# Kernel optimization log

Hardware: AMD Instinct MI355X
Metric: run time of the kernel (lower is better)

## Reference

```python
import jax, jax.numpy as jnp
import numpy as np

B, L, H, NB, D, DH = 8, 4096, 16, 8, 1024, 128

def setup_inputs() -> dict:
    key = jax.random.key(0)
    ks = jax.random.split(key, 12)
    theta_path = jax.random.normal(ks[0], (B, L, H, NB), jnp.float32)
    content_emb = jax.random.normal(ks[1], (B, L, D), jnp.float32)
    s_in = 1.0 / np.sqrt(D).astype(np.float32)
    s_h = 1.0 / np.sqrt(DH).astype(np.float32)
    # log_R_head: Linear(D,128) -> GELU -> Linear(128, H*NB), last layer weight *0.01, bias 0
    r_w1 = jax.random.normal(ks[2], (D, DH), jnp.float32) * s_in
    r_b1 = jnp.zeros((DH,), jnp.float32)
    r_w2 = jax.random.normal(ks[3], (DH, H * NB), jnp.float32) * s_h * 0.01
    r_b2 = jnp.zeros((H * NB,), jnp.float32)
    # measure_head
    m_w1 = jax.random.normal(ks[4], (D, DH), jnp.float32) * s_in
    m_b1 = jax.random.normal(ks[5], (DH,), jnp.float32) * s_in
    m_w2 = jax.random.normal(ks[6], (DH, H * NB), jnp.float32) * s_h
    m_b2 = jax.random.normal(ks[7], (H * NB,), jnp.float32) * s_h
    log_Q = jnp.full((H, NB), -3.0, jnp.float32)
    log_R_avg = jnp.full((H, NB), 1.0, jnp.float32)
    return {"theta_path": theta_path, "content_emb": content_emb,
            "log_Q": log_Q, "log_R_avg": log_R_avg,
            "r_w1": r_w1, "r_b1": r_b1, "r_w2": r_w2, "r_b2": r_b2,
            "m_w1": m_w1, "m_b1": m_b1, "m_w2": m_w2, "m_b2": m_b2}

def _mlp(x, w1, b1, w2, b2):
    h = jax.nn.gelu(x @ w1 + b1, approximate=False)  # torch nn.GELU default = exact
    return h @ w2 + b2

def reference(theta_path, content_emb, log_Q, log_R_avg,
              r_w1, r_b1, r_w2, r_b2, m_w1, m_b1, m_w2, m_b2):
    b, l, h, nb = theta_path.shape
    log_R = jnp.clip(_mlp(content_emb, r_w1, r_b1, r_w2, r_b2).reshape(b, l, h, nb), -5.0, 5.0)
    R = jnp.exp(log_R)
    z = jnp.pi * jnp.tanh(_mlp(content_emb, m_w1, m_b1, m_w2, m_b2).reshape(b, l, h, nb))
    diff = z - theta_path
    nu = jnp.arctan2(jnp.sin(diff), jnp.cos(diff))  # wrap angle error to (-pi, pi]
    Q = jnp.exp(log_Q)
    Ravg = jnp.exp(log_R_avg)
    Pi_dare = 0.5 * (-Q + jnp.sqrt(Q * Q + 4.0 * Q * Ravg))  # [H, NB]
    Pi = jnp.broadcast_to(Pi_dare[None, None], (b, l, h, nb))
    K = Pi / jnp.maximum(Pi + R, 1e-8)
    alpha = 1.0 - K
    u = K * nu
    # affine associative scan over sequence dim: d_t = alpha_t * d_{t-1} + u_t
    def combine(c1, c2):
        a1, u1 = c1
        a2, u2 = c2
        return (a2 * a1, a2 * u1 + u2)
    _, d = jax.lax.associative_scan(combine, (alpha, u), axis=1)
    return (theta_path + d, Pi, K, R)
```

## Files before the change

### kernel.cpp

```cpp
#include <hip/hip_runtime.h>
#include <hip/hip_bf16.h>
#include <cstdint>
#include <cstddef>

#define TOK 32768
#define CCH 128
#define DIN 1024

typedef __attribute__((ext_vector_type(8))) short short8;
typedef __attribute__((ext_vector_type(4))) float f32x4;

#define LIST_CAP 262144u

static __device__ __forceinline__ uint16_t f2bf(float f) {
  __hip_bfloat16 h = __float2bfloat16(f);
  return __builtin_bit_cast(uint16_t, h);
}
static __device__ __forceinline__ float bf2f(uint16_t u) {
  __hip_bfloat16 h = __builtin_bit_cast(__hip_bfloat16, u);
  return __bfloat162float(h);
}
static __device__ __forceinline__ void splitbf(float x, uint16_t& hi, uint16_t& lo) {
  hi = f2bf(x);
  lo = f2bf(x - bf2f(hi));
}

__global__ void prep_kernel(const float* __restrict__ r_w1, const float* __restrict__ r_w2,
                            const float* __restrict__ m_w1, const float* __restrict__ m_w2,
                            const float* __restrict__ logQ, const float* __restrict__ logRavg,
                            uint16_t* __restrict__ W1r, uint16_t* __restrict__ W2r,
                            uint16_t* __restrict__ W1mh, uint16_t* __restrict__ W1ml,
                            uint16_t* __restrict__ W2mh, uint16_t* __restrict__ W2ml,
                            float* __restrict__ PiArr, unsigned int* __restrict__ cnt)
{
  int idx = blockIdx.x * 256 + threadIdx.x;
  if (idx == 0) cnt[0] = 0;
  if (idx < 131072) {
    int e = idx;
    int j = e & 7, lane = (e >> 3) & 63, nt = (e >> 9) & 7, c = (e >> 12) & 1, kt = e >> 13;
    int k = kt * 64 + c * 32 + (lane >> 4) * 8 + j;
    int n = nt * 16 + (lane & 15);
    W1r[e] = f2bf(r_w1[k * 128 + n]);
  } else if (idx < 147456) {
    int e = idx - 131072;
    int j = e & 7, l = (e >> 3) & 63, c = (e >> 9) & 3, t = e >> 11;
    int k = c * 32 + (l >> 4) * 8 + j;
    int col = t * 16 + (l & 15);
    W2r[e] = f2bf(r_w2[k * 128 + col]);
  } else if (idx < 278528) {
    int e = idx - 147456;
    int j = e & 7, lane = (e >> 3) & 63, nt = (e >> 9) & 7, c = (e >> 12) & 1, kt = e >> 13;
    int k = kt * 64 + c * 32 + (lane >> 4) * 8 + j;
    int n = nt * 16 + (lane & 15);
    uint16_t h, l;
    splitbf(m_w1[k * 128 + n], h, l);
    W1mh[e] = h; W1ml[e] = l;
  } else if (idx < 294912) {
    int e = idx - 278528;
    int j = e & 7, l = (e >> 3) & 63, c = (e >> 9) & 3, t = e >> 11;
    int k = c * 32 + (l >> 4) * 8 + j;
    int col = t * 16 + (l & 15);
    uint16_t h, lo;
    splitbf(m_w2[k * 128 + col], h, lo);
    W2mh[e] = h; W2ml[e] = lo;
  } else if (idx < 295040) {
    int i = idx - 294912;
    float Q = expf(logQ[i]);
    float Rv = expf(logRavg[i]);
    PiArr[i] = 0.5f * (-Q + sqrtf(Q * Q + 4.0f * Q * Rv));
  }
}

__global__ __launch_bounds__(1024, 8) void fused_all(
    const float* __restrict__ X, const float* __restrict__ theta,
    const uint16_t* __restrict__ W1r, const uint16_t* __restrict__ W2r,
    const uint16_t* __restrict__ W1h, const uint16_t* __restrict__ W1l,
    const uint16_t* __restrict__ W2h, const uint16_t* __restrict__ W2l,
    const float* __restrict__ rB1, const float* __restrict__ rB2,
    const float* __restrict__ B1, const float* __restrict__ B2,
    const float* __restrict__ PiArr,
    float* __restrict__ out0, float* __restrict__ out1,
    float* __restrict__ out2, float* __restrict__ out3,
    float* __restrict__ AggA, float* __restrict__ AggU,
    unsigned int* __restrict__ cnt, unsigned int* __restrict__ list)
{
  union SM {
    struct { uint16_t Xh[2][64][72]; uint16_t Xl[2][64][72]; } s1;
    struct { uint16_t Hh[64][136]; uint16_t Hl[64][136]; uint16_t Hr[64][136]; } s2;
    struct { float2 Agg[4][4][128]; } s3;
  };
  __shared__ SM sm;

  const int tid = threadIdx.x;
  const int w = tid >> 6, lane = tid & 63;
  const int l15 = lane & 15, l4 = lane >> 4;
  const int tm = w >> 2, tn = w & 3;
  const int tok0 = blockIdx.x * 64;

  f32x4 accm[2], accr[2];
#pragma unroll
  for (int t = 0; t < 2; ++t) { accm[t] = 0.0f; accr[t] = 0.0f; }

  const int rr = tid >> 4, cc = tid & 15;
  float4 xv0;

  auto stageLoad = [&](int kt) {
    xv0 = *reinterpret_cast<const float4*>(
        X + (size_t)(tok0 + rr) * DIN + kt * 64 + cc * 4);
  };
  auto stageWrite = [&](int b) {
    ushort4 vh, vl;
    splitbf(xv0.x, vh.x, vl.x);
    splitbf(xv0.y, vh.y, vl.y);
    splitbf(xv0.z, vh.z, vl.z);
    splitbf(xv0.w, vh.w, vl.w);
    *reinterpret_cast<ushort4*>(&sm.s1.Xh[b][rr][cc * 4]) = vh;
    *reinterpret_cast<ushort4*>(&sm.s1.Xl[b][rr][cc * 4]) = vl;
  };

  stageLoad(0);
  stageWrite(0);
  __syncthreads();

  for (int kt = 0; kt < 16; ++kt) {
    const int cur = kt & 1;
    if (kt < 15) stageLoad(kt + 1);

    short8 bh[2][2], bl[2][2], br[2][2];
#pragma unroll
    for (int c = 0; c < 2; ++c)
#pragma unroll
      for (int t = 0; t < 2; ++t) {
        const size_t boff = (size_t)((((kt * 2 + c) * 8 + (tn * 2 + t)) * 64 + lane) * 8);
        bh[c][t] = *reinterpret_cast<const short8*>(W1h + boff);
        bl[c][t] = *reinterpret_cast<const short8*>(W1l + boff);
        br[c][t] = *reinterpret_cast<const short8*>(W1r + boff);
      }

#pragma unroll
    for (int c = 0; c < 2; ++c) {
      const int ko = c * 32 + l4 * 8;
      const int row = tm * 16 + l15;
      short8 ah = *reinterpret_cast<const short8*>(&sm.s1.Xh[cur][row][ko]);
      short8 al = *reinterpret_cast<const short8*>(&sm.s1.Xl[cur][row][ko]);
#pragma unroll
      for (int t = 0; t < 2; ++t) {
        accm[t] = __builtin_amdgcn_mfma_f32_16x16x32_bf16(ah, bh[c][t], accm[t], 0, 0, 0);
        accm[t] = __builtin_amdgcn_mfma_f32_16x16x32_bf16(al, bh[c][t], accm[t], 0, 0, 0);
        accm[t] = __builtin_amdgcn_mfma_f32_16x16x32_bf16(ah, bl[c][t], accm[t], 0, 0, 0);
        accr[t] = __builtin_amdgcn_mfma_f32_16x16x32_bf16(ah, br[c][t], accr[t], 0, 0, 0);
      }
    }

    if (kt < 15) stageWrite(cur ^ 1);
    __syncthreads();
  }

#pragma unroll
  for (int t = 0; t < 2; ++t) {
    const int n = (tn * 2 + t) * 16 + l15;
    const float b1m = B1[n];
    const float b1rr = rB1[n];
#pragma unroll
    for (int r = 0; r < 4; ++r) {
      const int row = tm * 16 + l4 * 4 + r;
      const float v = accm[t][r] + b1m;
      const float ev = erff(v / 1.41421356237309515f);
      const float g = 0.5f * v * (ev + 1.0f);
      uint16_t gh, gl;
      splitbf(g, gh, gl);
      sm.s2.Hh[row][n] = gh;
      sm.s2.Hl[row][n] = gl;
      const float vr = accr[t][r] + b1rr;
      const float gr = 0.5f * vr * (1.0f + erff(vr * 0.70710678118654752f));
      sm.s2.Hr[row][n] = f2bf(gr);
    }
  }
  __syncthreads();

  f32x4 acc2m[2], acc2r[2];
#pragma unroll
  for (int t = 0; t < 2; ++t) { acc2m[t] = 0.0f; acc2r[t] = 0.0f; }

#pragma unroll
  for (int c2 = 0; c2 < 4; ++c2) {
    const int ko = c2 * 32 + l4 * 8;
    const int row = tm * 16 + l15;
    short8 ah = *reinterpret_cast<const short8*>(&sm.s2.Hh[row][ko]);
    short8 al = *reinterpret_cast<const short8*>(&sm.s2.Hl[row][ko]);
    short8 ar = *reinterpret_cast<const short8*>(&sm.s2.Hr[row][ko]);
    short8 b2h[2], b2l[2], b2r[2];
#pragma unroll
    for (int t = 0; t < 2; ++t) {
      const size_t boff = (size_t)((((tn * 2 + t) * 4 + c2) * 64 + lane) * 8);
      b2h[t] = *reinterpret_cast<const short8*>(W2h + boff);
      b2l[t] = *reinterpret_cast<const short8*>(W2l + boff);
      b2r[t] = *reinterpret_cast<const short8*>(W2r + boff);
    }
#pragma unroll
    for (int t = 0; t < 2; ++t) {
      acc2m[t] = __builtin_amdgcn_mfma_f32_16x16x32_bf16(ah, b2h[t], acc2m[t], 0, 0, 0);
      acc2m[t] = __builtin_amdgcn_mfma_f32_16x16x32_bf16(al, b2h[t], acc2m[t], 0, 0, 0);
      acc2m[t] = __builtin_amdgcn_mfma_f32_16x16x32_bf16(ah, b2l[t], acc2m[t], 0, 0, 0);
      acc2r[t] = __builtin_amdgcn_mfma_f32_16x16x32_bf16(ar, b2r[t], acc2r[t], 0, 0, 0);
    }
  }

#pragma unroll
  for (int t = 0; t < 2; ++t) {
    const int n = (tn * 2 + t) * 16 + l15;
    const float b2 = rB2[n];
    const float piv = PiArr[n];
#pragma unroll
    for (int r = 0; r < 4; ++r) {
      const int token = tok0 + tm * 16 + l4 * 4 + r;
      float lr = acc2r[t][r] + b2;
      lr = fminf(fmaxf(lr, -5.0f), 5.0f);
      const float R = expf(lr);
      const float K = piv / fmaxf(piv + R, 1e-8f);
      const size_t off = (size_t)token * CCH + n;
      out1[off] = piv;
      out2[off] = K;
      out3[off] = R;
      acc2r[t][r] = K;
    }
  }

#pragma unroll
  for (int t = 0; t < 2; ++t) {
    const int n = (tn * 2 + t) * 16 + l15;
    const float b2 = B2[n];
#pragma unroll
    for (int r = 0; r < 4; ++r) {
      const int token = tok0 + tm * 16 + l4 * 4 + r;
      const float mz = acc2m[t][r] + b2;
      const float z = 3.14159265358979323846f * tanhf(mz);
      const float d = z - theta[(size_t)token * CCH + n];
      const float wr = d - 6.2831853071795864769f * rintf(d * 0.15915494309189533577f);
      if (3.14159265358979323846f - fabsf(wr) < 3e-4f) {
        unsigned int p = atomicAdd(cnt, 1u);
        if (p < LIST_CAP) list[p] = (unsigned int)(token * CCH + n);
      }
      out0[(size_t)token * CCH + n] = wr;
      acc2m[t][r] = wr;
    }
  }

  __syncthreads();
#pragma unroll
  for (int t = 0; t < 2; ++t) {
    const int n = (tn * 2 + t) * 16 + l15;
    float A = 1.0f, U = 0.0f;
#pragma unroll
    for (int r = 0; r < 4; ++r) {
      const float k = acc2r[t][r];
      const float v = acc2m[t][r];
      const float a = 1.0f - k;
      A *= a;
      U = fmaf(a, U, k * v);
    }
    sm.s3.Agg[tm][l4][n] = make_float2(A, U);
  }
  __syncthreads();
  if (tid < 128) {
    const int ch = tid;
    float A = 1.0f, U = 0.0f;
#pragma unroll
    for (int g = 0; g < 16; ++g) {
      const float2 au = sm.s3.Agg[g >> 2][g & 3][ch];
      U = fmaf(au.x, U, au.y);
      A *= au.x;
    }
    AggA[blockIdx.x * CCH + ch] = A;
    AggU[blockIdx.x * CCH + ch] = U;
  }
}

__global__ __launch_bounds__(128) void refine_nu(
    const float* __restrict__ X, const float* __restrict__ theta,
    const float* __restrict__ W1, const float* __restrict__ B1,
    const float* __restrict__ W2, const float* __restrict__ B2,
    const unsigned int* __restrict__ cnt, const unsigned int* __restrict__ list,
    float* __restrict__ out0)
{
  __shared__ float h[128];
  const int j = threadIdx.x;
  const unsigned int n = min(cnt[0], LIST_CAP);
  for (unsigned int e = blockIdx.x; e < n; e += gridDim.x) {
    const unsigned int idx = list[e];
    const int tok = (int)(idx >> 7), ch = (int)(idx & 127);
    const float* xr = X + (size_t)tok * DIN;
    float acc = 0.0f;
    for (int k = 0; k < DIN; ++k)
      acc = fmaf(xr[k], W1[(size_t)k * CCH + j], acc);
    const float v = acc + B1[j];
    const float ev = erff(v / 1.41421356237309515f);
    h[j] = 0.5f * v * (ev + 1.0f);
    __syncthreads();
    if (j == 0) {
      float a2 = 0.0f;
      for (int k = 0; k < CCH; ++k)
        a2 = fmaf(h[k], W2[(size_t)k * CCH + ch], a2);
      const float mz = a2 + B2[ch];
      const float z = 3.14159265358979323846f * tanhf(mz);
      const float d = z - theta[(size_t)tok * CCH + ch];
      out0[(size_t)tok * CCH + ch] = atan2f(sinf(d), cosf(d));
    }
    __syncthreads();
  }
}

__global__ __launch_bounds__(64) void refine_agg(
    const float* __restrict__ Kk, const float* __restrict__ nu,
    const unsigned int* __restrict__ cnt, const unsigned int* __restrict__ list,
    float* __restrict__ AggA, float* __restrict__ AggU)
{
  __shared__ float av[64], uv[64];
  const int i = threadIdx.x;
  const unsigned int n = min(cnt[0], LIST_CAP);
  for (unsigned int e = blockIdx.x; e < n; e += gridDim.x) {
    const unsigned int idx = list[e];
    const int ch = (int)(idx & 127);
    const int blk = (int)(idx >> 13);
    const size_t off = (size_t)(blk * 64 + i) * CCH + ch;
    const float k = Kk[off];
    const float v = nu[off];
    av[i] = 1.0f - k;
    uv[i] = k * v;
    __syncthreads();
    if (i == 0) {
      float A = 1.0f, U = 0.0f;
      for (int g = 0; g < 64; ++g) {
        U = fmaf(av[g], U, uv[g]);
        A *= av[g];
      }
      AggA[blk * CCH + ch] = A;
      AggU[blk * CCH + ch] = U;
    }
    __syncthreads();
  }
}

__global__ __launch_bounds__(256) void scan_pass2(
    const float* __restrict__ AggA, const float* __restrict__ AggU,
    float* __restrict__ Carry)
{
  const int wid = blockIdx.x * 4 + (threadIdx.x >> 6);
  const int b = wid >> 7, ch = wid & 127;
  const int g = threadIdx.x & 63;
  const size_t idx = (size_t)(b * 64 + g) * CCH + ch;
  float A = AggA[idx];
  float U = AggU[idx];
#pragma unroll
  for (int s = 1; s < 64; s <<= 1) {
    const float pA = __shfl_up(A, s);
    const float pU = __shfl_up(U, s);
    if (g >= s) {
      U = fmaf(A, pU, U);
      A = A * pA;
    }
  }
  float cU = __shfl_up(U, 1);
  if (g == 0) cU = 0.0f;
  Carry[idx] = cU;
}

__global__ __launch_bounds__(128) void scan_pass3(
    const float* __restrict__ Kk, const float* __restrict__ theta,
    const float* __restrict__ Carry, float* __restrict__ out0)
{
  __shared__ float kb[64 * CCH];
  __shared__ float vb[64 * CCH];
  const int c = threadIdx.x;
  const int blk = blockIdx.x;
  const size_t base = (size_t)blk * 64 * CCH;
#pragma unroll
  for (int i = 0; i < 16; ++i) {
    const int e = i * 128 + c;
    reinterpret_cast<float4*>(kb)[e] = reinterpret_cast<const float4*>(Kk + base)[e];
    reinterpret_cast<float4*>(vb)[e] = reinterpret_cast<const float4*>(out0 + base)[e];
  }
  __syncthreads();
  float d = Carry[blk * CCH + c];
#pragma unroll 8
  for (int i = 0; i < 64; ++i) {
    const float k = kb[i * CCH + c];
    const float v = vb[i * CCH + c];
    d = fmaf(1.0f - k, d, k * v);
    const size_t off = base + (size_t)i * CCH + c;
    out0[off] = theta[off] + d;
  }
}

extern "C" void kernel_launch(void* const* d_in, const int* in_sizes, int n_in,
                              void* d_out, int out_size, void* d_ws, size_t ws_size,
                              hipStream_t stream) {
  const float* theta   = (const float*)d_in[0];
  const float* X       = (const float*)d_in[1];
  const float* logQ    = (const float*)d_in[2];
  const float* logRavg = (const float*)d_in[3];
  const float* r_w1    = (const float*)d_in[4];
  const float* r_b1    = (const float*)d_in[5];
  const float* r_w2    = (const float*)d_in[6];
  const float* r_b2    = (const float*)d_in[7];
  const float* m_w1    = (const float*)d_in[8];
  const float* m_b1    = (const float*)d_in[9];
  const float* m_w2    = (const float*)d_in[10];
  const float* m_b2    = (const float*)d_in[11];

  float* out0 = (float*)d_out;
  float* out1 = out0 + 4194304;
  float* out2 = out0 + 2 * 4194304;
  float* out3 = out0 + 3 * 4194304;

  char* ws = (char*)d_ws;
  uint16_t* W1r  = (uint16_t*)(ws);
  uint16_t* W2r  = (uint16_t*)(ws + 262144);
  float* PiArr   = (float*)(ws + 295936);
  float* AggA    = (float*)(ws + 296448);
  float* AggU    = (float*)(ws + 558592);
  float* Carry   = (float*)(ws + 820736);
  unsigned int* cnt  = (unsigned int*)(ws + 1082880);
  unsigned int* list = (unsigned int*)(ws + 1083136);
  uint16_t* W1mh = (uint16_t*)(ws + 2131712);
  uint16_t* W1ml = (uint16_t*)(ws + 2393856);
  uint16_t* W2mh = (uint16_t*)(ws + 2656000);
  uint16_t* W2ml = (uint16_t*)(ws + 2688768);

  prep_kernel<<<1153, 256, 0, stream>>>(r_w1, r_w2, m_w1, m_w2, logQ, logRavg,
                                        W1r, W2r, W1mh, W1ml, W2mh, W2ml,
                                        PiArr, cnt);
  fused_all<<<512, 1024, 0, stream>>>(X, theta, W1r, W2r, W1mh, W1ml, W2mh, W2ml,
                                      r_b1, r_b2, m_b1, m_b2, PiArr,
                                      out0, out1, out2, out3, AggA, AggU, cnt, list);
  refine_nu<<<1024, 128, 0, stream>>>(X, theta, m_w1, m_b1, m_w2, m_b2,
                                      cnt, list, out0);
  refine_agg<<<1024, 64, 0, stream>>>(out2, out0, cnt, list, AggA, AggU);
  scan_pass2<<<256, 256, 0, stream>>>(AggA, AggU, Carry);
  scan_pass3<<<512, 128, 0, stream>>>(out2, theta, Carry, out0);
}
```

Before: 140.7 us.

## Remap fused MLP to 8 waves each owning one N-tile across all rows

```diff
diff --git a/kernel.cpp b/kernel.cpp
--- a/kernel.cpp
+++ b/kernel.cpp
@@ -71,7 +71,7 @@
   }
 }
 
-__global__ __launch_bounds__(1024, 8) void fused_all(
+__global__ __launch_bounds__(512, 4) void fused_all(
     const float* __restrict__ X, const float* __restrict__ theta,
     const uint16_t* __restrict__ W1r, const uint16_t* __restrict__ W2r,
     const uint16_t* __restrict__ W1h, const uint16_t* __restrict__ W1l,
@@ -94,172 +94,181 @@
   const int tid = threadIdx.x;
   const int w = tid >> 6, lane = tid & 63;
   const int l15 = lane & 15, l4 = lane >> 4;
-  const int tm = w >> 2, tn = w & 3;
+  const int tn = w;
   const int tok0 = blockIdx.x * 64;
 
-  f32x4 accm[2], accr[2];
-#pragma unroll
-  for (int t = 0; t < 2; ++t) { accm[t] = 0.0f; accr[t] = 0.0f; }
+  f32x4 accm[4], accr[4];
+#pragma unroll
+  for (int m = 0; m < 4; ++m) { accm[m] = 0.0f; accr[m] = 0.0f; }
 
   const int rr = tid >> 4, cc = tid & 15;
-  float4 xv0;
-
-  auto stageLoad = [&](int kt) {
-    xv0 = *reinterpret_cast<const float4*>(
+  float4 xa0, xa1, xb0, xb1;
+
+  auto ldX = [&](int kt, float4& v0, float4& v1) {
+    v0 = *reinterpret_cast<const float4*>(
         X + (size_t)(tok0 + rr) * DIN + kt * 64 + cc * 4);
+    v1 = *reinterpret_cast<const float4*>(
+        X + (size_t)(tok0 + rr + 32) * DIN + kt * 64 + cc * 4);
   };
-  auto stageWrite = [&](int b) {
+  auto wrX = [&](int b, const float4& v0, const float4& v1) {
     ushort4 vh, vl;
-    splitbf(xv0.x, vh.x, vl.x);
-    splitbf(xv0.y, vh.y, vl.y);
-    splitbf(xv0.z, vh.z, vl.z);
-    splitbf(xv0.w, vh.w, vl.w);
+    splitbf(v0.x, vh.x, vl.x);
+    splitbf(v0.y, vh.y, vl.y);
+    splitbf(v0.z, vh.z, vl.z);
+    splitbf(v0.w, vh.w, vl.w);
     *reinterpret_cast<ushort4*>(&sm.s1.Xh[b][rr][cc * 4]) = vh;
     *reinterpret_cast<ushort4*>(&sm.s1.Xl[b][rr][cc * 4]) = vl;
+    splitbf(v1.x, vh.x, vl.x);
+    splitbf(v1.y, vh.y, vl.y);
+    splitbf(v1.z, vh.z, vl.z);
+    splitbf(v1.w, vh.w, vl.w);
+    *reinterpret_cast<ushort4*>(&sm.s1.Xh[b][rr + 32][cc * 4]) = vh;
+    *reinterpret_cast<ushort4*>(&sm.s1.Xl[b][rr + 32][cc * 4]) = vl;
   };
 
-  stageLoad(0);
-  stageWrite(0);
+  ldX(0, xa0, xa1);
+  wrX(0, xa0, xa1);
+  ldX(1, xa0, xa1);
   __syncthreads();
 
+#pragma unroll
   for (int kt = 0; kt < 16; ++kt) {
     const int cur = kt & 1;
-    if (kt < 15) stageLoad(kt + 1);
-
-    short8 bh[2][2], bl[2][2], br[2][2];
-#pragma unroll
-    for (int c = 0; c < 2; ++c)
-#pragma unroll
-      for (int t = 0; t < 2; ++t) {
-        const size_t boff = (size_t)((((kt * 2 + c) * 8 + (tn * 2 + t)) * 64 + lane) * 8);
-        bh[c][t] = *reinterpret_cast<const short8*>(W1h + boff);
-        bl[c][t] = *reinterpret_cast<const short8*>(W1l + boff);
-        br[c][t] = *reinterpret_cast<const short8*>(W1r + boff);
-      }
+
+    short8 bh[2], bl[2], br[2];
+#pragma unroll
+    for (int c = 0; c < 2; ++c) {
+      const size_t boff = (size_t)((((kt * 2 + c) * 8 + tn) * 64 + lane) * 8);
+      bh[c] = *reinterpret_cast<const short8*>(W1h + boff);
+      bl[c] = *reinterpret_cast<const short8*>(W1l + boff);
+      br[c] = *reinterpret_cast<const short8*>(W1r + boff);
+    }
+    if (kt < 14) ldX(kt + 2, xb0, xb1);
 
 #pragma unroll
     for (int c = 0; c < 2; ++c) {
       const int ko = c * 32 + l4 * 8;
-      const int row = tm * 16 + l15;
-      short8 ah = *reinterpret_cast<const short8*>(&sm.s1.Xh[cur][row][ko]);
-      short8 al = *reinterpret_cast<const short8*>(&sm.s1.Xl[cur][row][ko]);
-#pragma unroll
-      for (int t = 0; t < 2; ++t) {
-        accm[t] = __builtin_amdgcn_mfma_f32_16x16x32_bf16(ah, bh[c][t], accm[t], 0, 0, 0);
-        accm[t] = __builtin_amdgcn_mfma_f32_16x16x32_bf16(al, bh[c][t], accm[t], 0, 0, 0);
-        accm[t] = __builtin_amdgcn_mfma_f32_16x16x32_bf16(ah, bl[c][t], accm[t], 0, 0, 0);
-        accr[t] = __builtin_amdgcn_mfma_f32_16x16x32_bf16(ah, br[c][t], accr[t], 0, 0, 0);
+#pragma unroll
+      for (int m = 0; m < 4; ++m) {
+        const int row = m * 16 + l15;
+        const short8 ah = *reinterpret_cast<const short8*>(&sm.s1.Xh[cur][row][ko]);
+        const short8 al = *reinterpret_cast<const short8*>(&sm.s1.Xl[cur][row][ko]);
+        accm[m] = __builtin_amdgcn_mfma_f32_16x16x32_bf16(ah, bh[c], accm[m], 0, 0, 0);
+        accm[m] = __builtin_amdgcn_mfma_f32_16x16x32_bf16(al, bh[c], accm[m], 0, 0, 0);
+        accm[m] = __builtin_amdgcn_mfma_f32_16x16x32_bf16(ah, bl[c], accm[m], 0, 0, 0);
+        accr[m] = __builtin_amdgcn_mfma_f32_16x16x32_bf16(ah, br[c], accr[m], 0, 0, 0);
       }
     }
 
-    if (kt < 15) stageWrite(cur ^ 1);
+    if (kt < 15) { wrX(cur ^ 1, xa0, xa1); xa0 = xb0; xa1 = xb1; }
     __syncthreads();
   }
 
-#pragma unroll
-  for (int t = 0; t < 2; ++t) {
-    const int n = (tn * 2 + t) * 16 + l15;
+  short8 b2h[4], b2l[4], b2r[4];
+#pragma unroll
+  for (int c2 = 0; c2 < 4; ++c2) {
+    const size_t boff = (size_t)(((tn * 4 + c2) * 64 + lane) * 8);
+    b2h[c2] = *reinterpret_cast<const short8*>(W2h + boff);
+    b2l[c2] = *reinterpret_cast<const short8*>(W2l + boff);
+    b2r[c2] = *reinterpret_cast<const short8*>(W2r + boff);
+  }
+
+  const int n = tn * 16 + l15;
+  {
     const float b1m = B1[n];
     const float b1rr = rB1[n];
 #pragma unroll
-    for (int r = 0; r < 4; ++r) {
-      const int row = tm * 16 + l4 * 4 + r;
-      const float v = accm[t][r] + b1m;
-      const float ev = erff(v / 1.41421356237309515f);
-      const float g = 0.5f * v * (ev + 1.0f);
-      uint16_t gh, gl;
-      splitbf(g, gh, gl);
-      sm.s2.Hh[row][n] = gh;
-      sm.s2.Hl[row][n] = gl;
-      const float vr = accr[t][r] + b1rr;
-      const float gr = 0.5f * vr * (1.0f + erff(vr * 0.70710678118654752f));
-      sm.s2.Hr[row][n] = f2bf(gr);
-    }
+    for (int m = 0; m < 4; ++m)
+#pragma unroll
+      for (int r = 0; r < 4; ++r) {
+        const int row = m * 16 + l4 * 4 + r;
+        const float v = accm[m][r] + b1m;
+        const float ev = erff(v / 1.41421356237309515f);
+        const float g = 0.5f * v * (ev + 1.0f);
+        uint16_t gh, gl;
+        splitbf(g, gh, gl);
+        sm.s2.Hh[row][n] = gh;
+        sm.s2.Hl[row][n] = gl;
+        const float vr = accr[m][r] + b1rr;
+        const float gr = 0.5f * vr * (1.0f + erff(vr * 0.70710678118654752f));
+        sm.s2.Hr[row][n] = f2bf(gr);
+      }
   }
   __syncthreads();
 
-  f32x4 acc2m[2], acc2r[2];
-#pragma unroll
-  for (int t = 0; t < 2; ++t) { acc2m[t] = 0.0f; acc2r[t] = 0.0f; }
+  f32x4 acc2m[4], acc2r[4];
+#pragma unroll
+  for (int m = 0; m < 4; ++m) { acc2m[m] = 0.0f; acc2r[m] = 0.0f; }
 
 #pragma unroll
   for (int c2 = 0; c2 < 4; ++c2) {
     const int ko = c2 * 32 + l4 * 8;
-    const int row = tm * 16 + l15;
-    short8 ah = *reinterpret_cast<const short8*>(&sm.s2.Hh[row][ko]);
-    short8 al = *reinterpret_cast<const short8*>(&sm.s2.Hl[row][ko]);
-    short8 ar = *reinterpret_cast<const short8*>(&sm.s2.Hr[row][ko]);
-    short8 b2h[2], b2l[2], b2r[2];
-#pragma unroll
-    for (int t = 0; t < 2; ++t) {
-      const size_t boff = (size_t)((((tn * 2 + t) * 4 + c2) * 64 + lane) * 8);
-      b2h[t] = *reinterpret_cast<const short8*>(W2h + boff);
-      b2l[t] = *reinterpret_cast<const short8*>(W2l + boff);
-      b2r[t] = *reinterpret_cast<const short8*>(W2r + boff);
-    }
-#pragma unroll
-    for (int t = 0; t < 2; ++t) {
-      acc2m[t] = __builtin_amdgcn_mfma_f32_16x16x32_bf16(ah, b2h[t], acc2m[t], 0, 0, 0);
-      acc2m[t] = __builtin_amdgcn_mfma_f32_16x16x32_bf16(al, b2h[t], acc2m[t], 0, 0, 0);
-      acc2m[t] = __builtin_amdgcn_mfma_f32_16x16x32_bf16(ah, b2l[t], acc2m[t], 0, 0, 0);
-      acc2r[t] = __builtin_amdgcn_mfma_f32_16x16x32_bf16(ar, b2r[t], acc2r[t], 0, 0, 0);
-    }
-  }
-
-#pragma unroll
-  for (int t = 0; t < 2; ++t) {
-    const int n = (tn * 2 + t) * 16 + l15;
+#pragma unroll
+    for (int m = 0; m < 4; ++m) {
+      const int row = m * 16 + l15;
+      const short8 ah = *reinterpret_cast<const short8*>(&sm.s2.Hh[row][ko]);
+      const short8 al = *reinterpret_cast<const short8*>(&sm.s2.Hl[row][ko]);
+      const short8 ar = *reinterpret_cast<const short8*>(&sm.s2.Hr[row][ko]);
+      acc2m[m] = __builtin_amdgcn_mfma_f32_16x16x32_bf16(ah, b2h[c2], acc2m[m], 0, 0, 0);
+      acc2m[m] = __builtin_amdgcn_mfma_f32_16x16x32_bf16(al, b2h[c2], acc2m[m], 0, 0, 0);
+      acc2m[m] = __builtin_amdgcn_mfma_f32_16x16x32_bf16(ah, b2l[c2], acc2m[m], 0, 0, 0);
+      acc2r[m] = __builtin_amdgcn_mfma_f32_16x16x32_bf16(ar, b2r[c2], acc2r[m], 0, 0, 0);
+    }
+  }
+
+  {
     const float b2 = rB2[n];
     const float piv = PiArr[n];
 #pragma unroll
+    for (int m = 0; m < 4; ++m)
+#pragma unroll
+      for (int r = 0; r < 4; ++r) {
+        const int token = tok0 + m * 16 + l4 * 4 + r;
+        float lr = acc2r[m][r] + b2;
+        lr = fminf(fmaxf(lr, -5.0f), 5.0f);
+        const float R = expf(lr);
+        const float K = piv / fmaxf(piv + R, 1e-8f);
+        const size_t off = (size_t)token * CCH + n;
+        out1[off] = piv;
+        out2[off] = K;
+        out3[off] = R;
+        acc2r[m][r] = K;
+      }
+  }
+
+  {
+    const float b2 = B2[n];
+#pragma unroll
+    for (int m = 0; m < 4; ++m)
+#pragma unroll
+      for (int r = 0; r < 4; ++r) {
+        const int token = tok0 + m * 16 + l4 * 4 + r;
+        const float mz = acc2m[m][r] + b2;
+        const float z = 3.14159265358979323846f * tanhf(mz);
+        const float d = z - theta[(size_t)token * CCH + n];
+        const float wr = d - 6.2831853071795864769f * rintf(d * 0.15915494309189533577f);
+        if (3.14159265358979323846f - fabsf(wr) < 3e-4f) {
+          unsigned int p = atomicAdd(cnt, 1u);
+          if (p < LIST_CAP) list[p] = (unsigned int)(token * CCH + n);
+        }
+        out0[(size_t)token * CCH + n] = wr;
+        acc2m[m][r] = wr;
+      }
+  }
+
+  __syncthreads();
+#pragma unroll
+  for (int m = 0; m < 4; ++m) {
+    float A = 1.0f, U = 0.0f;
+#pragma unroll
     for (int r = 0; r < 4; ++r) {
-      const int token = tok0 + tm * 16 + l4 * 4 + r;
-      float lr = acc2r[t][r] + b2;
-      lr = fminf(fmaxf(lr, -5.0f), 5.0f);
-      const float R = expf(lr);
-      const float K = piv / fmaxf(piv + R, 1e-8f);
-      const size_t off = (size_t)token * CCH + n;
-      out1[off] = piv;
-      out2[off] = K;
-      out3[off] = R;
-      acc2r[t][r] = K;
-    }
-  }
-
-#pragma unroll
-  for (int t = 0; t < 2; ++t) {
-    const int n = (tn * 2 + t) * 16 + l15;
-    const float b2 = B2[n];
-#pragma unroll
-    for (int r = 0; r < 4; ++r) {
-      const int token = tok0 + tm * 16 + l4 * 4 + r;
-      const float mz = acc2m[t][r] + b2;
-      const float z = 3.14159265358979323846f * tanhf(mz);
-      const float d = z - theta[(size_t)token * CCH + n];
-      const float wr = d - 6.2831853071795864769f * rintf(d * 0.15915494309189533577f);
-      if (3.14159265358979323846f - fabsf(wr) < 3e-4f) {
-        unsigned int p = atomicAdd(cnt, 1u);
-        if (p < LIST_CAP) list[p] = (unsigned int)(token * CCH + n);
-      }
-      out0[(size_t)token * CCH + n] = wr;
-      acc2m[t][r] = wr;
-    }
-  }
-
-  __syncthreads();
-#pragma unroll
-  for (int t = 0; t < 2; ++t) {
-    const int n = (tn * 2 + t) * 16 + l15;
-    float A = 1.0f, U = 0.0f;
-#pragma unroll
-    for (int r = 0; r < 4; ++r) {
-      const float k = acc2r[t][r];
-      const float v = acc2m[t][r];
+      const float k = acc2r[m][r];
+      const float v = acc2m[m][r];
       const float a = 1.0f - k;
       A *= a;
       U = fmaf(a, U, k * v);
     }
-    sm.s3.Agg[tm][l4][n] = make_float2(A, U);
+    sm.s3.Agg[m][l4][n] = make_float2(A, U);
   }
   __syncthreads();
   if (tid < 128) {
@@ -430,9 +439,9 @@
   prep_kernel<<<1153, 256, 0, stream>>>(r_w1, r_w2, m_w1, m_w2, logQ, logRavg,
                                         W1r, W2r, W1mh, W1ml, W2mh, W2ml,
                                         PiArr, cnt);
-  fused_all<<<512, 1024, 0, stream>>>(X, theta, W1r, W2r, W1mh, W1ml, W2mh, W2ml,
-                                      r_b1, r_b2, m_b1, m_b2, PiArr,
-                                      out0, out1, out2, out3, AggA, AggU, cnt, list);
+  fused_all<<<512, 512, 0, stream>>>(X, theta, W1r, W2r, W1mh, W1ml, W2mh, W2ml,
+                                     r_b1, r_b2, m_b1, m_b2, PiArr,
+                                     out0, out1, out2, out3, AggA, AggU, cnt, list);
   refine_nu<<<1024, 128, 0, stream>>>(X, theta, m_w1, m_b1, m_w2, m_b2,
                                       cnt, list, out0);
   refine_agg<<<1024, 64, 0, stream>>>(out2, out0, cnt, list, AggA, AggU);
```

New measurement: 123.4 us. -12.3%, faster.
